# Optimization experiments

Measured on AMD Instinct MI355X. Metric: run time of the kernel, lower is better.

Reference implementation:

```python
import jax, jax.numpy as jnp
import numpy as np

B, E, D, NH, NP = 4, 32, 1024, 16, 4
LQ = E * E
DH = D // NH


def layer_norm(x, g, b, eps=1e-6):
    m = x.mean(-1, keepdims=True)
    v = ((x - m) ** 2).mean(-1, keepdims=True)
    return (x - m) / jnp.sqrt(v + eps) * g + b


def get_ref(H, W):
    # matches MSCrossAttnBlock.get_reference_points: centers normalized to [0,1], (x, y) order
    ys, xs = jnp.meshgrid((jnp.arange(H, dtype=jnp.float32) + 0.5) / H,
                          (jnp.arange(W, dtype=jnp.float32) + 0.5) / W, indexing='ij')
    return jnp.stack([xs.ravel(), ys.ravel()], -1)  # (H*W, 2)


def bilinear_sample(value_l, loc, H, W):
    # value_l: (N, nH, H*W, dh); loc: (N, Lq, nH, P, 2) normalized to [0,1]
    # replicates F.grid_sample(align_corners=False, padding_mode='zeros') with grid = 2*loc - 1
    N, Lq, nH, P, _ = loc.shape
    x = loc[..., 0] * W - 0.5
    y = loc[..., 1] * H - 0.5
    x0 = jnp.floor(x)
    y0 = jnp.floor(y)
    wx1 = x - x0
    wy1 = y - y0
    out = 0.0
    for dy, wy in ((0, 1.0 - wy1), (1, wy1)):
        for dx, wx in ((0, 1.0 - wx1), (1, wx1)):
            xi = x0 + dx
            yi = y0 + dy
            valid = (xi >= 0) & (xi < W) & (yi >= 0) & (yi < H)
            idx = (jnp.clip(yi, 0, H - 1) * W + jnp.clip(xi, 0, W - 1)).astype(jnp.int32)
            idx_t = idx.transpose(0, 2, 1, 3).reshape(N, nH, Lq * P)  # (N, nH, Lq*P)
            g = jnp.take_along_axis(value_l, idx_t[..., None], axis=2)  # (N, nH, Lq*P, dh)
            g = g.reshape(N, nH, Lq, P, -1).transpose(0, 2, 1, 3, 4)  # (N, Lq, nH, P, dh)
            w = (wx * wy) * valid.astype(value_l.dtype)
            out = out + g * w[..., None]
    return out


def msdeform(query, ref, inp, shapes, Wv, bv, Wo, bo, Wa, ba, Wp, bp):
    # MSDeformAttn forward (no padding mask)
    N, Lq, d = query.shape
    nL = len(shapes)
    value = (inp @ Wv.T + bv).reshape(N, -1, NH, DH).transpose(0, 2, 1, 3)  # (N, nH, Lin, dh)
    off = (query @ Wo.T + bo).reshape(N, Lq, NH, nL, NP, 2)
    attw = jax.nn.softmax((query @ Wa.T + ba).reshape(N, Lq, NH, nL * NP), axis=-1)
    attw = attw.reshape(N, Lq, NH, nL, NP)
    normalizer = jnp.array([[w, h] for (h, w) in shapes], dtype=query.dtype)  # (nL, 2) = [W, H]
    loc = ref[None, :, None, None, None, :] + off / normalizer[None, None, None, :, None, :]
    out = 0.0
    start = 0
    for l, (H, W) in enumerate(shapes):
        sampled = bilinear_sample(value[:, :, start:start + H * W], loc[:, :, :, l], H, W)
        out = out + (sampled * attw[:, :, :, l, :, None]).sum(3)  # (N, Lq, nH, dh)
        start += H * W
    return out.reshape(N, Lq, d) @ Wp.T + bp


def setup_inputs() -> dict:
    key = jax.random.key(0)
    ks = iter(jax.random.split(key, 64))
    def rnd(shape, scale):
        return jax.random.normal(next(ks), shape, dtype=jnp.float32) * scale
    inp = {}
    for i in range(4):
        inp[f'src{i}'] = rnd((B, LQ, D), 1.0)
    for nm in ('qn', 'fn', 'n1'):
        inp[nm + '_g'] = jnp.ones((D,), jnp.float32)
        inp[nm + '_b'] = jnp.zeros((D,), jnp.float32)
    inp['gamma1'] = rnd((D,), 0.1)
    inp['gamma2'] = rnd((D,), 0.1)
    ws = D ** -0.5
    for pre, nl in (('ca', 4), ('sa', 1)):
        inp[pre + '_vw'] = rnd((D, D), ws)
        inp[pre + '_vb'] = jnp.zeros((D,), jnp.float32)
        inp[pre + '_ow'] = rnd((NH * nl * NP * 2, D), ws)
        inp[pre + '_ob'] = rnd((NH * nl * NP * 2,), 0.1)
        inp[pre + '_aw'] = rnd((NH * nl * NP, D), ws)
        inp[pre + '_ab'] = jnp.zeros((NH * nl * NP,), jnp.float32)
        inp[pre + '_pw'] = rnd((D, D), ws)
        inp[pre + '_pb'] = jnp.zeros((D,), jnp.float32)
    return inp


def reference(src0, src1, src2, src3, qn_g, qn_b, fn_g, fn_b, n1_g, n1_b, gamma1, gamma2,
              ca_vw, ca_vb, ca_ow, ca_ob, ca_aw, ca_ab, ca_pw, ca_pb,
              sa_vw, sa_vb, sa_ow, sa_ob, sa_aw, sa_ab, sa_pw, sa_pb):
    shapes4 = [(E, E)] * 4
    feat = jnp.concatenate([src0, src1, src2, src3], axis=1)  # (B, 4*LQ, D)
    query = src3  # srcs[-1], pos embed is None
    ref = get_ref(E, E)  # (LQ, 2)
    attn = msdeform(layer_norm(query, qn_g, qn_b), ref, layer_norm(feat, fn_g, fn_b),
                    shapes4, ca_vw, ca_vb, ca_ow, ca_ob, ca_aw, ca_ab, ca_pw, ca_pb)
    attn1 = layer_norm(attn, n1_g, n1_b)
    attn2 = msdeform(attn1, ref, attn1, [(E, E)],
                     sa_vw, sa_vb, sa_ow, sa_ob, sa_aw, sa_ab, sa_pw, sa_pb)
    attn = attn + gamma2 * attn2
    return query + gamma1 * attn
```

## Files before the change

### kernel.cpp

```cpp
#include <hip/hip_runtime.h>


#define DEV __device__ __forceinline__

typedef float f32x4 __attribute__((ext_vector_type(4)));
typedef __bf16 bf16x8 __attribute__((ext_vector_type(8)));

DEV unsigned short f2bf(float f) {
  union { float f; unsigned u; } a; a.f = f;
  unsigned r = a.u + 0x7fffu + ((a.u >> 16) & 1u);
  return (unsigned short)(r >> 16);
}
DEV float bf2f(unsigned short h) {
  union { unsigned u; float f; } a; a.u = ((unsigned)h) << 16;
  return a.f;
}

struct CvtArgs {
  const float* src[8];
  unsigned short* dst;
  int off4[9];
};

__global__ __launch_bounds__(256) void f2bf_multi(CvtArgs a) {
  int i = blockIdx.x * 256 + threadIdx.x;
  int seg = 0;
  #pragma unroll
  for (int s = 1; s < 8; ++s) seg += (i >= a.off4[s]) ? 1 : 0;
  const float4 v = ((const float4*)a.src[seg])[i - a.off4[seg]];
  unsigned short* o = a.dst + (size_t)i * 4;
  o[0] = f2bf(v.x); o[1] = f2bf(v.y); o[2] = f2bf(v.z); o[3] = f2bf(v.w);
}

DEV void ln_row_wave(const float* __restrict__ xr, const float* __restrict__ g,
                     const float* __restrict__ b,
                     unsigned short* __restrict__ op_row) {
  const int lane = threadIdx.x & 63;
  float4 v[4];
  float s = 0.f, s2 = 0.f;
  #pragma unroll
  for (int j = 0; j < 4; ++j) {
    v[j] = ((const float4*)xr)[lane + 64 * j];
    s  += v[j].x + v[j].y + v[j].z + v[j].w;
    s2 += v[j].x*v[j].x + v[j].y*v[j].y + v[j].z*v[j].z + v[j].w*v[j].w;
  }
  #pragma unroll
  for (int o = 32; o; o >>= 1) { s += __shfl_xor(s, o); s2 += __shfl_xor(s2, o); }
  const float mean = s * (1.f / 1024.f);
  const float rstd = rsqrtf(s2 * (1.f / 1024.f) - mean * mean + 1e-6f);
  #pragma unroll
  for (int j = 0; j < 4; ++j) {
    float4 gg = ((const float4*)g)[lane + 64 * j];
    float4 bb = ((const float4*)b)[lane + 64 * j];
    ushort4 r;
    r.x = f2bf((v[j].x - mean) * rstd * gg.x + bb.x);
    r.y = f2bf((v[j].y - mean) * rstd * gg.y + bb.y);
    r.z = f2bf((v[j].z - mean) * rstd * gg.z + bb.z);
    r.w = f2bf((v[j].w - mean) * rstd * gg.w + bb.w);
    ((ushort4*)op_row)[lane + 64 * j] = r;
  }
}

__global__ __launch_bounds__(256) void ln_wave_kernel(
    const float* __restrict__ x, const float* __restrict__ g,
    const float* __restrict__ b, unsigned short* __restrict__ out) {
  int row = blockIdx.x * 4 + (threadIdx.x >> 6);
  ln_row_wave(x + (size_t)row * 1024, g, b, out + (size_t)row * 1024);
}

__global__ __launch_bounds__(256) void ln5_wave_kernel(
    const float* __restrict__ s0, const float* __restrict__ s1,
    const float* __restrict__ s2, const float* __restrict__ s3,
    const float* __restrict__ fg, const float* __restrict__ fb,
    const float* __restrict__ qg, const float* __restrict__ qb,
    unsigned short* __restrict__ f_out, unsigned short* __restrict__ q_out) {
  int row = blockIdx.x * 4 + (threadIdx.x >> 6);
  if (row < 16384) {
    int l = row >> 12, inner = row & 4095;
    const float* srcs[4] = {s0, s1, s2, s3};
    int orow = (inner >> 10) * 4096 + l * 1024 + (inner & 1023);
    ln_row_wave(srcs[l] + (size_t)inner * 1024, fg, fb,
                f_out + (size_t)orow * 1024);
  } else {
    int inner = row - 16384;
    ln_row_wave(s3 + (size_t)inner * 1024, qg, qb,
                q_out + (size_t)inner * 1024);
  }
}

struct GemmP {
  const unsigned short* A; const unsigned short* W;
  void* C; void* C1; void* C2;
  const float* b0; const float* b1; const float* b2;
  const float* src3; const float* g1; const float* g2; const float* attnp;
  int M, N, K, tilesM;
};

template <int BM, int BN, int EPI>
DEV void gemm_body(const GemmP& P, int id, unsigned short* sA,
                   unsigned short* sB) {
  constexpr int WMT = BM / 2, WNT = BN / 2;
  constexpr int MF = WMT / 16, NF = WNT / 16;
  constexpr int PA = BM / 64, PB = BN / 64;
  const int tid = threadIdx.x;
  const int wave = tid >> 6, lane = tid & 63;
  const int wm = (wave & 1) * WMT, wn = (wave >> 1) * WNT;
  const int m0 = (id % P.tilesM) * BM;
  const int n0 = (id / P.tilesM) * BN;
  const int lq = lane >> 4, lm = lane & 15;
  const int r16 = lane >> 2;
  const int cst = lane & 3;
  const int csrc = cst ^ ((r16 >> 1) & 3);
  const int aslot = lq ^ ((lm >> 1) & 3);

  f32x4 acc[MF][NF] = {};
  bf16x8 ald[2][PA], bld[2][PB];

  #pragma unroll 1
  for (int k0 = 0; k0 < P.K; k0 += 64) {
    #pragma unroll
    for (int s = 0; s < 2; ++s) {
      #pragma unroll
      for (int p = 0; p < PA; ++p) {
        int grow = m0 + (wave + 4 * p) * 16 + r16;
        ald[s][p] = *(const bf16x8*)(P.A + (size_t)grow * P.K + k0 + s * 32 + csrc * 8);
      }
      #pragma unroll
      for (int p = 0; p < PB; ++p) {
        int grow = min(n0 + (wave + 4 * p) * 16 + r16, P.N - 1);
        bld[s][p] = *(const bf16x8*)(P.W + (size_t)grow * P.K + k0 + s * 32 + csrc * 8);
      }
    }
    __syncthreads();
    #pragma unroll
    for (int s = 0; s < 2; ++s) {
      #pragma unroll
      for (int p = 0; p < PA; ++p)
        *(bf16x8*)(sA + s * BM * 32 + (wave + 4 * p) * 512 + (r16 * 4 + cst) * 8) = ald[s][p];
      #pragma unroll
      for (int p = 0; p < PB; ++p)
        *(bf16x8*)(sB + s * BN * 32 + (wave + 4 * p) * 512 + (r16 * 4 + cst) * 8) = bld[s][p];
    }
    __syncthreads();
    #pragma unroll
    for (int s = 0; s < 2; ++s) {
      bf16x8 af[MF], bfr[NF];
      #pragma unroll
      for (int mi = 0; mi < MF; ++mi)
        af[mi] = *(const bf16x8*)(sA + s * BM * 32 + ((wm >> 4) + mi) * 512 + lm * 32 + aslot * 8);
      #pragma unroll
      for (int ni = 0; ni < NF; ++ni)
        bfr[ni] = *(const bf16x8*)(sB + s * BN * 32 + ((wn >> 4) + ni) * 512 + lm * 32 + aslot * 8);
      #pragma unroll
      for (int mi = 0; mi < MF; ++mi)
        #pragma unroll
        for (int ni = 0; ni < NF; ++ni)
          acc[mi][ni] = __builtin_amdgcn_mfma_f32_16x16x32_bf16(
              af[mi], bfr[ni], acc[mi][ni], 0, 0, 0);
    }
  }

  #pragma unroll
  for (int mi = 0; mi < MF; ++mi) {
    #pragma unroll
    for (int ni = 0; ni < NF; ++ni) {
      const int col = n0 + wn + ni * 16 + lm;
      #pragma unroll
      for (int r2 = 0; r2 < 4; ++r2) {
        const int row = m0 + wm + mi * 16 + lq * 4 + r2;
        float v = acc[mi][ni][r2];
        if constexpr (EPI == 0) {
          ((float*)P.C)[(size_t)row * 1024 + col] = v + P.b0[col];
        } else if constexpr (EPI == 1) {
          ((unsigned short*)P.C)[(size_t)row * 1024 + col] = f2bf(v + P.b0[col]);
        } else if constexpr (EPI == 2) {
          if (col < 512)
            ((float*)P.C)[(size_t)row * 512 + col] = v + P.b0[col];
          else
            ((float*)P.C1)[(size_t)row * 256 + col - 512] = v + P.b1[col - 512];
        } else if constexpr (EPI == 3) {
          if (col < 1024)
            ((unsigned short*)P.C)[(size_t)row * 1024 + col] = f2bf(v + P.b0[col]);
          else if (col < 1152)
            ((float*)P.C1)[(size_t)row * 128 + col - 1024] = v + P.b1[col - 1024];
          else if (col < 1216)
            ((float*)P.C2)[(size_t)row * 64 + col - 1152] = v + P.b2[col - 1152];
        } else {
          size_t i = (size_t)row * 1024 + col;
          float vv = v + P.b0[col];
          ((float*)P.C)[i] = P.src3[i] + P.g1[col] * (P.attnp[i] + P.g2[col] * vv);
        }
      }
    }
  }
}

template <int BM, int BN, int EPI>
__global__ __launch_bounds__(256) void gemm_v3(GemmP P) {
  extern __shared__ __align__(16) unsigned short smem[];
  gemm_body<BM, BN, EPI>(P, blockIdx.x, smem, smem + BM * 64);
}

template <int BM, int BN>
__global__ __launch_bounds__(256) void gemm_dual(GemmP Pv, GemmP Po, int split) {
  extern __shared__ __align__(16) unsigned short smem[];
  if ((int)blockIdx.x < split)
    gemm_body<BM, BN, 1>(Pv, blockIdx.x, smem, smem + BM * 64);
  else
    gemm_body<BM, BN, 2>(Po, blockIdx.x - split, smem, smem + BM * 64);
}

template <int NLEV>
__global__ __launch_bounds__(256) void ms_sample_fused(
    const unsigned short* __restrict__ value, const float* __restrict__ off,
    const float* __restrict__ logits, unsigned short* __restrict__ out) {
  const int nq = blockIdx.x;
  const int wave = threadIdx.x >> 6, lane = threadIdx.x & 63;
  const int h = (wave << 2) + (lane >> 4);
  const int c = (lane & 15) << 2;
  const int q = nq & 1023, n = nq >> 10;
  const float* offp = off + ((size_t)nq * 16 + h) * (NLEV * 8);
  const float* lgp  = logits + ((size_t)nq * 16 + h) * (NLEV * 4);

  float lg[NLEV * 4];
  #pragma unroll
  for (int i = 0; i < NLEV; ++i) {
    float4 v = ((const float4*)lgp)[i];
    lg[4*i] = v.x; lg[4*i+1] = v.y; lg[4*i+2] = v.z; lg[4*i+3] = v.w;
  }
  float mx = lg[0];
  #pragma unroll
  for (int i = 1; i < NLEV * 4; ++i) mx = fmaxf(mx, lg[i]);
  float ssum = 0.f;
  #pragma unroll
  for (int i = 0; i < NLEV * 4; ++i) { lg[i] = __expf(lg[i] - mx); ssum += lg[i]; }
  const float inv = 1.f / ssum;

  const float fqx = (float)(q & 31), fqy = (float)(q >> 5);
  float a0 = 0.f, a1 = 0.f, a2 = 0.f, a3 = 0.f;

  #pragma unroll
  for (int l = 0; l < NLEV; ++l) {
    const unsigned short* vl =
        value + ((size_t)(n * NLEV + l) << 20) + h * 64 + c;
    #pragma unroll
    for (int p = 0; p < 4; ++p) {
      float2 o2 = ((const float2*)offp)[l * 4 + p];
      float aw = lg[l * 4 + p] * inv;
      float xx = fqx + o2.x, yy = fqy + o2.y;
      float xf = floorf(xx), yf = floorf(yy);
      float fx = xx - xf, fy = yy - yf;
      int ix = (int)xf, iy = (int)yf;
      int ix1 = ix + 1, iy1 = iy + 1;
      float vx0 = ((unsigned)ix  < 32u) ? 1.f : 0.f;
      float vx1 = ((unsigned)ix1 < 32u) ? 1.f : 0.f;
      float vy0 = ((unsigned)iy  < 32u) ? 1.f : 0.f;
      float vy1 = ((unsigned)iy1 < 32u) ? 1.f : 0.f;
      int cx0 = min(max(ix, 0), 31), cx1 = min(max(ix1, 0), 31);
      int cy0 = min(max(iy, 0), 31), cy1 = min(max(iy1, 0), 31);
      float w00 = (1.f - fx) * (1.f - fy) * vx0 * vy0 * aw;
      float w01 = fx * (1.f - fy) * vx1 * vy0 * aw;
      float w10 = (1.f - fx) * fy * vx0 * vy1 * aw;
      float w11 = fx * fy * vx1 * vy1 * aw;
      ushort4 u00 = *(const ushort4*)(vl + ((size_t)(cy0 * 32 + cx0) << 10));
      ushort4 u01 = *(const ushort4*)(vl + ((size_t)(cy0 * 32 + cx1) << 10));
      ushort4 u10 = *(const ushort4*)(vl + ((size_t)(cy1 * 32 + cx0) << 10));
      ushort4 u11 = *(const ushort4*)(vl + ((size_t)(cy1 * 32 + cx1) << 10));
      a0 += w00 * bf2f(u00.x) + w01 * bf2f(u01.x) + w10 * bf2f(u10.x) + w11 * bf2f(u11.x);
      a1 += w00 * bf2f(u00.y) + w01 * bf2f(u01.y) + w10 * bf2f(u10.y) + w11 * bf2f(u11.y);
      a2 += w00 * bf2f(u00.z) + w01 * bf2f(u01.z) + w10 * bf2f(u10.z) + w11 * bf2f(u11.z);
      a3 += w00 * bf2f(u00.w) + w01 * bf2f(u01.w) + w10 * bf2f(u10.w) + w11 * bf2f(u11.w);
    }
  }
  ushort4 r;
  r.x = f2bf(a0); r.y = f2bf(a1); r.z = f2bf(a2); r.w = f2bf(a3);
  *(ushort4*)(out + ((size_t)nq * 16 + h) * 64 + c) = r;
}

extern "C" void kernel_launch(void* const* d_in, const int* in_sizes, int n_in,
                              void* d_out, int out_size, void* d_ws,
                              size_t ws_size, hipStream_t stream) {
  (void)in_sizes; (void)n_in; (void)out_size; (void)ws_size;
  const float* src[4] = {(const float*)d_in[0], (const float*)d_in[1],
                         (const float*)d_in[2], (const float*)d_in[3]};
  const float* qn_g = (const float*)d_in[4];
  const float* qn_b = (const float*)d_in[5];
  const float* fn_g = (const float*)d_in[6];
  const float* fn_b = (const float*)d_in[7];
  const float* n1_g = (const float*)d_in[8];
  const float* n1_b = (const float*)d_in[9];
  const float* gamma1 = (const float*)d_in[10];
  const float* gamma2 = (const float*)d_in[11];
  const float* ca_vw = (const float*)d_in[12];
  const float* ca_vb = (const float*)d_in[13];
  const float* ca_ow = (const float*)d_in[14];
  const float* ca_ob = (const float*)d_in[15];
  const float* ca_aw = (const float*)d_in[16];
  const float* ca_ab = (const float*)d_in[17];
  const float* ca_pw = (const float*)d_in[18];
  const float* ca_pb = (const float*)d_in[19];
  const float* sa_vw = (const float*)d_in[20];
  const float* sa_vb = (const float*)d_in[21];
  const float* sa_ow = (const float*)d_in[22];
  const float* sa_ob = (const float*)d_in[23];
  const float* sa_aw = (const float*)d_in[24];
  const float* sa_ab = (const float*)d_in[25];
  const float* sa_pw = (const float*)d_in[26];
  const float* sa_pb = (const float*)d_in[27];

  char* wsp = (char*)d_ws;
  size_t off = 0;
  auto alloc = [&](size_t bytes) {
    char* r = wsp + off;
    off = (off + bytes + 255) & ~(size_t)255;
    return r;
  };
  const size_t MB = 1024 * 1024;
  unsigned short* w_ca_vw = (unsigned short*)alloc(1024 * 1024 * 2);
  unsigned short* w_ca_ow = (unsigned short*)alloc(512 * 1024 * 2);
  unsigned short* w_ca_aw = (unsigned short*)alloc(256 * 1024 * 2);
  unsigned short* w_ca_pw = (unsigned short*)alloc(1024 * 1024 * 2);
  unsigned short* w_sa_vw = (unsigned short*)alloc(1024 * 1024 * 2);
  unsigned short* w_sa_ow = (unsigned short*)alloc(128 * 1024 * 2);
  unsigned short* w_sa_aw = (unsigned short*)alloc(64 * 1024 * 2);
  unsigned short* w_sa_pw = (unsigned short*)alloc(1024 * 1024 * 2);
  (void)w_ca_aw; (void)w_sa_ow; (void)w_sa_aw;
  char* R1 = alloc(32 * MB);
  char* R2 = alloc(32 * MB);
  char* R3 = alloc(8 * MB);
  char* R4 = alloc(8 * MB);
  char* R5 = alloc(4 * MB);

  unsigned short* f_ln    = (unsigned short*)R1;
  float*          attn    = (float*)R1;
  unsigned short* attn1   = (unsigned short*)(R1 + 16 * MB);
  unsigned short* samp_sa = (unsigned short*)(R1 + 24 * MB);
  unsigned short* val_ca  = (unsigned short*)R2;
  unsigned short* val_sa  = (unsigned short*)R2;
  unsigned short* q_ln    = (unsigned short*)R3;
  unsigned short* samp_ca = (unsigned short*)R3;
  float*          off_ca  = (float*)R4;
  float*          off_sa  = (float*)R4;
  float*          attw_sa = (float*)(R4 + 4 * MB);
  float*          attw_ca = (float*)R5;

  CvtArgs ca;
  ca.src[0] = ca_vw; ca.src[1] = ca_ow; ca.src[2] = ca_aw; ca.src[3] = ca_pw;
  ca.src[4] = sa_vw; ca.src[5] = sa_ow; ca.src[6] = sa_aw; ca.src[7] = sa_pw;
  ca.dst = w_ca_vw;
  const int sizes4[8] = {262144, 131072, 65536, 262144, 262144, 32768, 16384, 262144};
  ca.off4[0] = 0;
  for (int i = 0; i < 8; ++i) ca.off4[i + 1] = ca.off4[i] + sizes4[i];
  f2bf_multi<<<ca.off4[8] / 256, 256, 0, stream>>>(ca);

  ln5_wave_kernel<<<5120, 256, 0, stream>>>(src[0], src[1], src[2], src[3],
                                            fn_g, fn_b, qn_g, qn_b, f_ln, q_ln);

  auto mkP = [](const unsigned short* A, const unsigned short* W, void* C,
                const float* b0, int M, int N, int K, int tilesM) {
    GemmP p{}; p.A = A; p.W = W; p.C = C; p.b0 = b0;
    p.M = M; p.N = N; p.K = K; p.tilesM = tilesM;
    return p;
  };

  {
    GemmP pv = mkP(f_ln, w_ca_vw, val_ca, ca_vb, 16384, 1024, 1024, 128);
    GemmP po = mkP(q_ln, w_ca_ow, off_ca, ca_ob, 4096, 768, 1024, 32);
    po.C1 = attw_ca; po.b1 = ca_ab;
    gemm_dual<128, 128><<<1024 + 192, 256, 65536 / 2, stream>>>(pv, po, 1024);
  }

  ms_sample_fused<4><<<4096, 256, 0, stream>>>(val_ca, off_ca, attw_ca, samp_ca);
  gemm_v3<64, 128, 0><<<64 * 8, 256, (64 + 128) * 64 * 2, stream>>>(
      mkP(samp_ca, w_ca_pw, attn, ca_pb, 4096, 1024, 1024, 64));

  ln_wave_kernel<<<1024, 256, 0, stream>>>(attn, n1_g, n1_b, attn1);
  {
    GemmP p = mkP(attn1, w_sa_vw, val_sa, sa_vb, 4096, 1216, 1024, 64);
    p.C1 = off_sa; p.b1 = sa_ob; p.C2 = attw_sa; p.b2 = sa_ab;
    gemm_v3<64, 128, 3><<<64 * 10, 256, (64 + 128) * 64 * 2, stream>>>(p);
  }
  ms_sample_fused<1><<<4096, 256, 0, stream>>>(val_sa, off_sa, attw_sa, samp_sa);
  {
    GemmP p = mkP(samp_sa, w_sa_pw, d_out, sa_pb, 4096, 1024, 1024, 64);
    p.src3 = src[3]; p.g1 = gamma1; p.g2 = gamma2; p.attnp = attn;
    gemm_v3<64, 128, 4><<<64 * 8, 256, (64 + 128) * 64 * 2, stream>>>(p);
  }
}
```

Baseline: 357.0 us.

## Use 32x32 MFMA tiles, fuse softmax into GEMM epilogue, merge prep kernels

The GEMM inner loop switches from 16x16x32 to 32x32x16 bf16 MFMA instructions, reorganising LDS fragment loads and the epilogue row mapping for the larger output fragment. The attention-weight softmax moves from the sampling kernel into the GEMM epilogue using cross-lane shuffles. The weight bf16 conversion and the layer-norm launch are merged into one prep kernel. Together these aim to raise MFMA throughput, drop redundant exp work per sampling lane and save a launch, at the cost of more accumulator registers per wave and a more intricate epilogue.

```diff
diff --git a/kernel.cpp b/kernel.cpp
--- a/kernel.cpp
+++ b/kernel.cpp
@@ -4,6 +4,7 @@
 #define DEV __device__ __forceinline__
 
 typedef float f32x4 __attribute__((ext_vector_type(4)));
+typedef float f32x16 __attribute__((ext_vector_type(16)));
 typedef __bf16 bf16x8 __attribute__((ext_vector_type(8)));
 
 DEV unsigned short f2bf(float f) {
@@ -21,16 +22,11 @@
   unsigned short* dst;
   int off4[9];
 };
-
-__global__ __launch_bounds__(256) void f2bf_multi(CvtArgs a) {
-  int i = blockIdx.x * 256 + threadIdx.x;
-  int seg = 0;
-  #pragma unroll
-  for (int s = 1; s < 8; ++s) seg += (i >= a.off4[s]) ? 1 : 0;
-  const float4 v = ((const float4*)a.src[seg])[i - a.off4[seg]];
-  unsigned short* o = a.dst + (size_t)i * 4;
-  o[0] = f2bf(v.x); o[1] = f2bf(v.y); o[2] = f2bf(v.z); o[3] = f2bf(v.w);
-}
+struct LnArgs {
+  const float* s[4];
+  const float* fg; const float* fb; const float* qg; const float* qb;
+  unsigned short* f_out; unsigned short* q_out;
+};
 
 DEV void ln_row_wave(const float* __restrict__ xr, const float* __restrict__ g,
                      const float* __restrict__ b,
@@ -61,31 +57,35 @@
   }
 }
 
+__global__ __launch_bounds__(256) void prep_kernel(CvtArgs a, LnArgs L) {
+  if (blockIdx.x < 5056) {
+    int i = blockIdx.x * 256 + threadIdx.x;
+    int seg = 0;
+    #pragma unroll
+    for (int s = 1; s < 8; ++s) seg += (i >= a.off4[s]) ? 1 : 0;
+    const float4 v = ((const float4*)a.src[seg])[i - a.off4[seg]];
+    unsigned short* o = a.dst + (size_t)i * 4;
+    o[0] = f2bf(v.x); o[1] = f2bf(v.y); o[2] = f2bf(v.z); o[3] = f2bf(v.w);
+  } else {
+    int row = (blockIdx.x - 5056) * 4 + (threadIdx.x >> 6);
+    if (row < 16384) {
+      int l = row >> 12, inner = row & 4095;
+      int orow = (inner >> 10) * 4096 + l * 1024 + (inner & 1023);
+      ln_row_wave(L.s[l] + (size_t)inner * 1024, L.fg, L.fb,
+                  L.f_out + (size_t)orow * 1024);
+    } else {
+      int inner = row - 16384;
+      ln_row_wave(L.s[3] + (size_t)inner * 1024, L.qg, L.qb,
+                  L.q_out + (size_t)inner * 1024);
+    }
+  }
+}
+
 __global__ __launch_bounds__(256) void ln_wave_kernel(
     const float* __restrict__ x, const float* __restrict__ g,
     const float* __restrict__ b, unsigned short* __restrict__ out) {
   int row = blockIdx.x * 4 + (threadIdx.x >> 6);
   ln_row_wave(x + (size_t)row * 1024, g, b, out + (size_t)row * 1024);
-}
-
-__global__ __launch_bounds__(256) void ln5_wave_kernel(
-    const float* __restrict__ s0, const float* __restrict__ s1,
-    const float* __restrict__ s2, const float* __restrict__ s3,
-    const float* __restrict__ fg, const float* __restrict__ fb,
-    const float* __restrict__ qg, const float* __restrict__ qb,
-    unsigned short* __restrict__ f_out, unsigned short* __restrict__ q_out) {
-  int row = blockIdx.x * 4 + (threadIdx.x >> 6);
-  if (row < 16384) {
-    int l = row >> 12, inner = row & 4095;
-    const float* srcs[4] = {s0, s1, s2, s3};
-    int orow = (inner >> 10) * 4096 + l * 1024 + (inner & 1023);
-    ln_row_wave(srcs[l] + (size_t)inner * 1024, fg, fb,
-                f_out + (size_t)orow * 1024);
-  } else {
-    int inner = row - 16384;
-    ln_row_wave(s3 + (size_t)inner * 1024, qg, qb,
-                q_out + (size_t)inner * 1024);
-  }
 }
 
 struct GemmP {
@@ -100,20 +100,20 @@
 DEV void gemm_body(const GemmP& P, int id, unsigned short* sA,
                    unsigned short* sB) {
   constexpr int WMT = BM / 2, WNT = BN / 2;
-  constexpr int MF = WMT / 16, NF = WNT / 16;
+  constexpr int MF2 = WMT / 32, NF2 = WNT / 32;
   constexpr int PA = BM / 64, PB = BN / 64;
   const int tid = threadIdx.x;
   const int wave = tid >> 6, lane = tid & 63;
   const int wm = (wave & 1) * WMT, wn = (wave >> 1) * WNT;
   const int m0 = (id % P.tilesM) * BM;
   const int n0 = (id / P.tilesM) * BN;
-  const int lq = lane >> 4, lm = lane & 15;
+  const int l32 = lane & 31, l16 = lane & 15, khalf = lane >> 5;
   const int r16 = lane >> 2;
   const int cst = lane & 3;
   const int csrc = cst ^ ((r16 >> 1) & 3);
-  const int aslot = lq ^ ((lm >> 1) & 3);
-
-  f32x4 acc[MF][NF] = {};
+  const int swz = (l16 >> 1) & 3;
+
+  f32x16 acc[MF2][NF2] = {};
   bf16x8 ald[2][PA], bld[2][PB];
 
   #pragma unroll 1
@@ -144,47 +144,75 @@
     __syncthreads();
     #pragma unroll
     for (int s = 0; s < 2; ++s) {
-      bf16x8 af[MF], bfr[NF];
-      #pragma unroll
-      for (int mi = 0; mi < MF; ++mi)
-        af[mi] = *(const bf16x8*)(sA + s * BM * 32 + ((wm >> 4) + mi) * 512 + lm * 32 + aslot * 8);
-      #pragma unroll
-      for (int ni = 0; ni < NF; ++ni)
-        bfr[ni] = *(const bf16x8*)(sB + s * BN * 32 + ((wn >> 4) + ni) * 512 + lm * 32 + aslot * 8);
-      #pragma unroll
-      for (int mi = 0; mi < MF; ++mi)
+      #pragma unroll
+      for (int t = 0; t < 2; ++t) {
+        const int kc = t * 2 + khalf;
+        const int slot = kc ^ swz;
+        bf16x8 af[MF2], bfr[NF2];
         #pragma unroll
-        for (int ni = 0; ni < NF; ++ni)
-          acc[mi][ni] = __builtin_amdgcn_mfma_f32_16x16x32_bf16(
-              af[mi], bfr[ni], acc[mi][ni], 0, 0, 0);
-    }
-  }
-
-  #pragma unroll
-  for (int mi = 0; mi < MF; ++mi) {
-    #pragma unroll
-    for (int ni = 0; ni < NF; ++ni) {
-      const int col = n0 + wn + ni * 16 + lm;
-      #pragma unroll
-      for (int r2 = 0; r2 < 4; ++r2) {
-        const int row = m0 + wm + mi * 16 + lq * 4 + r2;
-        float v = acc[mi][ni][r2];
+        for (int mi = 0; mi < MF2; ++mi) {
+          int ag = (wm >> 4) + mi * 2 + (l32 >> 4);
+          af[mi] = *(const bf16x8*)(sA + s * BM * 32 + ag * 512 + l16 * 32 + slot * 8);
+        }
+        #pragma unroll
+        for (int ni = 0; ni < NF2; ++ni) {
+          int bg = (wn >> 4) + ni * 2 + (l32 >> 4);
+          bfr[ni] = *(const bf16x8*)(sB + s * BN * 32 + bg * 512 + l16 * 32 + slot * 8);
+        }
+        #pragma unroll
+        for (int mi = 0; mi < MF2; ++mi)
+          #pragma unroll
+          for (int ni = 0; ni < NF2; ++ni)
+            acc[mi][ni] = __builtin_amdgcn_mfma_f32_32x32x16_bf16(
+                af[mi], bfr[ni], acc[mi][ni], 0, 0, 0);
+      }
+    }
+  }
+
+  #pragma unroll
+  for (int mi = 0; mi < MF2; ++mi) {
+    #pragma unroll
+    for (int ni = 0; ni < NF2; ++ni) {
+      const int colbase = n0 + wn + ni * 32;
+      const int col = colbase + l32;
+      #pragma unroll
+      for (int r = 0; r < 16; ++r) {
+        const int row = m0 + wm + mi * 32 + (r & 3) + 8 * (r >> 2) + 4 * khalf;
+        float v = acc[mi][ni][r];
         if constexpr (EPI == 0) {
           ((float*)P.C)[(size_t)row * 1024 + col] = v + P.b0[col];
         } else if constexpr (EPI == 1) {
           ((unsigned short*)P.C)[(size_t)row * 1024 + col] = f2bf(v + P.b0[col]);
         } else if constexpr (EPI == 2) {
-          if (col < 512)
+          if (colbase < 512) {
             ((float*)P.C)[(size_t)row * 512 + col] = v + P.b0[col];
-          else
-            ((float*)P.C1)[(size_t)row * 256 + col - 512] = v + P.b1[col - 512];
+          } else {
+            float x = v + P.b1[col - 512];
+            float m = x;
+            #pragma unroll
+            for (int o = 8; o; o >>= 1) m = fmaxf(m, __shfl_xor(m, o));
+            float e = __expf(x - m);
+            float ss = e;
+            #pragma unroll
+            for (int o = 8; o; o >>= 1) ss += __shfl_xor(ss, o);
+            ((float*)P.C1)[(size_t)row * 256 + col - 512] = e / ss;
+          }
         } else if constexpr (EPI == 3) {
-          if (col < 1024)
+          if (colbase < 1024) {
             ((unsigned short*)P.C)[(size_t)row * 1024 + col] = f2bf(v + P.b0[col]);
-          else if (col < 1152)
+          } else if (colbase < 1152) {
             ((float*)P.C1)[(size_t)row * 128 + col - 1024] = v + P.b1[col - 1024];
-          else if (col < 1216)
-            ((float*)P.C2)[(size_t)row * 64 + col - 1152] = v + P.b2[col - 1152];
+          } else if (colbase < 1216) {
+            float x = v + P.b2[col - 1152];
+            float m = x;
+            #pragma unroll
+            for (int o = 2; o; o >>= 1) m = fmaxf(m, __shfl_xor(m, o));
+            float e = __expf(x - m);
+            float ss = e;
+            #pragma unroll
+            for (int o = 2; o; o >>= 1) ss += __shfl_xor(ss, o);
+            ((float*)P.C2)[(size_t)row * 64 + col - 1152] = e / ss;
+          }
         } else {
           size_t i = (size_t)row * 1024 + col;
           float vv = v + P.b0[col];
@@ -213,28 +241,21 @@
 template <int NLEV>
 __global__ __launch_bounds__(256) void ms_sample_fused(
     const unsigned short* __restrict__ value, const float* __restrict__ off,
-    const float* __restrict__ logits, unsigned short* __restrict__ out) {
+    const float* __restrict__ attw, unsigned short* __restrict__ out) {
   const int nq = blockIdx.x;
   const int wave = threadIdx.x >> 6, lane = threadIdx.x & 63;
   const int h = (wave << 2) + (lane >> 4);
   const int c = (lane & 15) << 2;
   const int q = nq & 1023, n = nq >> 10;
   const float* offp = off + ((size_t)nq * 16 + h) * (NLEV * 8);
-  const float* lgp  = logits + ((size_t)nq * 16 + h) * (NLEV * 4);
+  const float* awp  = attw + ((size_t)nq * 16 + h) * (NLEV * 4);
 
   float lg[NLEV * 4];
   #pragma unroll
   for (int i = 0; i < NLEV; ++i) {
-    float4 v = ((const float4*)lgp)[i];
+    float4 v = ((const float4*)awp)[i];
     lg[4*i] = v.x; lg[4*i+1] = v.y; lg[4*i+2] = v.z; lg[4*i+3] = v.w;
   }
-  float mx = lg[0];
-  #pragma unroll
-  for (int i = 1; i < NLEV * 4; ++i) mx = fmaxf(mx, lg[i]);
-  float ssum = 0.f;
-  #pragma unroll
-  for (int i = 0; i < NLEV * 4; ++i) { lg[i] = __expf(lg[i] - mx); ssum += lg[i]; }
-  const float inv = 1.f / ssum;
 
   const float fqx = (float)(q & 31), fqy = (float)(q >> 5);
   float a0 = 0.f, a1 = 0.f, a2 = 0.f, a3 = 0.f;
@@ -246,7 +267,7 @@
     #pragma unroll
     for (int p = 0; p < 4; ++p) {
       float2 o2 = ((const float2*)offp)[l * 4 + p];
-      float aw = lg[l * 4 + p] * inv;
+      float aw = lg[l * 4 + p];
       float xx = fqx + o2.x, yy = fqy + o2.y;
       float xf = floorf(xx), yf = floorf(yy);
       float fx = xx - xf, fy = yy - yf;
@@ -351,10 +372,11 @@
   const int sizes4[8] = {262144, 131072, 65536, 262144, 262144, 32768, 16384, 262144};
   ca.off4[0] = 0;
   for (int i = 0; i < 8; ++i) ca.off4[i + 1] = ca.off4[i] + sizes4[i];
-  f2bf_multi<<<ca.off4[8] / 256, 256, 0, stream>>>(ca);
-
-  ln5_wave_kernel<<<5120, 256, 0, stream>>>(src[0], src[1], src[2], src[3],
-                                            fn_g, fn_b, qn_g, qn_b, f_ln, q_ln);
+  LnArgs la;
+  la.s[0] = src[0]; la.s[1] = src[1]; la.s[2] = src[2]; la.s[3] = src[3];
+  la.fg = fn_g; la.fb = fn_b; la.qg = qn_g; la.qb = qn_b;
+  la.f_out = f_ln; la.q_out = q_ln;
+  prep_kernel<<<10176, 256, 0, stream>>>(ca, la);
 
   auto mkP = [](const unsigned short* A, const unsigned short* W, void* C,
                 const float* b0, int M, int N, int K, int tilesM) {
@@ -367,7 +389,7 @@
     GemmP pv = mkP(f_ln, w_ca_vw, val_ca, ca_vb, 16384, 1024, 1024, 128);
     GemmP po = mkP(q_ln, w_ca_ow, off_ca, ca_ob, 4096, 768, 1024, 32);
     po.C1 = attw_ca; po.b1 = ca_ab;
-    gemm_dual<128, 128><<<1024 + 192, 256, 65536 / 2, stream>>>(pv, po, 1024);
+    gemm_dual<128, 128><<<1024 + 192, 256, 32768, stream>>>(pv, po, 1024);
   }
 
   ms_sample_fused<4><<<4096, 256, 0, stream>>>(val_ca, off_ca, attw_ca, samp_ca);
```

Result: slower. 390.4 us (+9.4%).
